# Kernel optimization log

Hardware: AMD Instinct MI355X
Metric: run time of the kernel (lower is better)

## Reference

```python
import jax, jax.numpy as jnp
import numpy as np

B, N, E, H = 8, 512, 64, 128


def setup_inputs() -> dict:
    key = jax.random.key(0)
    ks = jax.random.split(key, 9)
    s_in = 1.0 / np.sqrt(2 * E)
    s_h = 1.0 / np.sqrt(H)
    s_e = 1.0 / np.sqrt(E)
    return {
        "X": jax.random.normal(ks[0], (B, N, E), dtype=jnp.float32),
        # cross-sim MLP: Linear(2E,H) -> ReLU -> Linear(H,1) -> Sigmoid
        "Wc1": jax.random.uniform(ks[1], (2 * E, H), jnp.float32, -s_in, s_in),
        "bc1": jax.random.uniform(ks[2], (H,), jnp.float32, -s_in, s_in),
        "Wc2": jax.random.uniform(ks[3], (H, 1), jnp.float32, -s_h, s_h),
        "bc2": jax.random.uniform(ks[4], (1,), jnp.float32, -s_h, s_h),
        # self-sim MLP: Linear(E,H) -> ReLU -> Linear(H,1) -> Sigmoid
        "Ws1": jax.random.uniform(ks[5], (E, H), jnp.float32, -s_e, s_e),
        "bs1": jax.random.uniform(ks[6], (H,), jnp.float32, -s_e, s_e),
        "Ws2": jax.random.uniform(ks[7], (H, 1), jnp.float32, -s_h, s_h),
        "bs2": jax.random.uniform(ks[8], (1,), jnp.float32, -s_h, s_h),
    }


def reference(X, Wc1, bc1, Wc2, bc2, Ws1, bs1, Ws2, bs2):
    b, n, _ = X.shape
    idx_i, idx_j = jnp.triu_indices(n, k=1)  # [P], P = n(n-1)/2

    # gather pairwise features: [B, P, 2E]
    X_i = X[:, idx_i, :]
    X_j = X[:, idx_j, :]
    pair = jnp.concatenate([X_i, X_j], axis=-1)

    # tiny cross-sim MLP -> [B, P]
    h = jax.nn.relu(jnp.einsum("bpe,eh->bph", pair, Wc1) + bc1)
    sim_upper = jax.nn.sigmoid(jnp.einsum("bph,ho->bpo", h, Wc2) + bc2)[..., 0]

    # self-sim MLP on the diagonal -> [B, N]
    hd = jax.nn.relu(jnp.einsum("bne,eh->bnh", X, Ws1) + bs1)
    sim_diag = jax.nn.sigmoid(jnp.einsum("bnh,ho->bno", hd, Ws2) + bs2)[..., 0]

    # scatter into symmetric sim matrix [B, N, N]
    sim = jnp.zeros((b, n, n), dtype=X.dtype)
    sim = sim.at[:, idx_i, idx_j].set(sim_upper)
    sim = sim.at[:, idx_j, idx_i].set(sim_upper)
    diag = jnp.arange(n)
    sim = sim.at[:, diag, diag].set(sim_diag)
    return sim
```

## Files before the change

### kernel.cpp

```cpp
#include <hip/hip_runtime.h>

typedef float v4f __attribute__((ext_vector_type(4)));
typedef float v2f __attribute__((ext_vector_type(2)));

#define NTOK 512
#define EDIM 64
#define HDIM 128
#define NN   (NTOK*NTOK)

__device__ __forceinline__ float sigf(float x) {
    return __builtin_amdgcn_rcpf(1.f + __expf(-x));
}

__global__ __launch_bounds__(128) void precomp_kernel(
    const float* __restrict__ X, const float* __restrict__ Wc1, const float* __restrict__ bc1,
    const float* __restrict__ Ws1, const float* __restrict__ bs1,
    const float* __restrict__ Ws2, const float* __restrict__ bs2,
    float* __restrict__ Ag, float* __restrict__ Bg, float* __restrict__ out)
{
    __shared__ float Xs[8*EDIM];
    __shared__ float red[8*132];
    const int t  = threadIdx.x;
    const int g0 = blockIdx.x * 8;

    for (int i = t; i < 8*EDIM; i += 128) Xs[i] = X[g0*EDIM + i];
    __syncthreads();

    float accA[8] = {0}, accB[8] = {0}, accS[8] = {0};
    #pragma unroll 8
    for (int e = 0; e < EDIM; e++) {
        float wt = Wc1[e*HDIM + t];
        float wb = Wc1[(EDIM+e)*HDIM + t];
        float ws = Ws1[e*HDIM + t];
        #pragma unroll
        for (int r = 0; r < 8; r++) {
            float x = Xs[r*EDIM + e];
            accA[r] = fmaf(x, wt, accA[r]);
            accB[r] = fmaf(x, wb, accB[r]);
            accS[r] = fmaf(x, ws, accS[r]);
        }
    }
    const float b1 = bc1[t], s1 = bs1[t], w2 = Ws2[t];
    #pragma unroll
    for (int r = 0; r < 8; r++) {
        Ag[(g0+r)*HDIM + t] = accA[r];
        Bg[(g0+r)*HDIM + t] = accB[r] + b1;
        float hd = fmaxf(accS[r] + s1, 0.f);
        red[r*132 + t] = hd * w2;
    }
    __syncthreads();
    if (t < 8) {
        const float* rr = red + t*132;
        float s = 0.f;
        #pragma unroll
        for (int i = 0; i < HDIM/4; i++) {
            v4f v = *(const v4f*)(rr + 4*i);
            s += v[0] + v[1] + v[2] + v[3];
        }
        float val = sigf(s + bs2[0]);
        int g = g0 + t;
        int b = g >> 9, n = g & 511;
        out[b*NN + n*NTOK + n] = val;
    }
}

__global__ __launch_bounds__(256) void pair_kernel(
    const float* __restrict__ Ag, const float* __restrict__ Bg,
    const float* __restrict__ Wc2, const float* __restrict__ bc2,
    float* __restrict__ out)
{
    __shared__ float RowT[64*HDIM];
    __shared__ float ColT[32*HDIM];
    __shared__ float WcS[HDIM];

    const int t = threadIdx.x;
    const int b = blockIdx.y;
    const int u = blockIdx.x;
    int tr, tc, half;
    if (u < 56) {
        int p = u >> 1; half = u & 1;
        tr = 0; int rem = p;
        while (rem >= 7 - tr) { rem -= 7 - tr; tr++; }
        tc = tr + 1 + rem;
    } else {
        int d = (u - 56) >> 1; half = u & 1; tr = d; tc = d;
    }
    const int r0 = tr*64, c0 = tc*64 + half*32;
    const bool isdiag = (tr == tc);

    const float* Rsrc = Ag + (b*NTOK + r0)*HDIM;
    const float* Csrc = Bg + (b*NTOK + c0)*HDIM;

    if (t < 32) *(v4f*)(WcS + 4*t) = *(const v4f*)(Wc2 + 4*t);
    {
        const int hv = t & 31;
        for (int k = t >> 5; k < 64; k += 8) {
            const int sw = 4*(hv ^ (k & 31));
            *(v4f*)(RowT + k*HDIM + sw) = *(const v4f*)(Rsrc + k*HDIM + 4*hv);
        }
        for (int k = t >> 5; k < 32; k += 8) {
            const int sw = 4*(hv ^ k);
            *(v4f*)(ColT + k*HDIM + sw) = *(const v4f*)(Csrc + k*HDIM + 4*hv);
        }
    }
    __syncthreads();

    const int tj = t & 15, ti = t >> 4;
    int rbase[4], rmask[4];
    #pragma unroll
    for (int uu = 0; uu < 4; uu++) { int k = ti + 16*uu; rbase[uu] = k*HDIM; rmask[uu] = k & 31; }
    int cbase[2], cmask[2];
    #pragma unroll
    for (int v = 0; v < 2; v++) { int c = 2*tj + v; cbase[v] = c*HDIM; cmask[v] = c & 31; }

    float acc[4][2] = {};
    for (int hq = 0; hq < HDIM/4; hq++) {
        const v4f w4 = *(const v4f*)(WcS + 4*hq);
        v4f ra[4], cb[2];
        #pragma unroll
        for (int uu = 0; uu < 4; uu++) ra[uu] = *(const v4f*)(RowT + rbase[uu] + 4*(hq ^ rmask[uu]));
        #pragma unroll
        for (int v = 0; v < 2; v++)   cb[v]  = *(const v4f*)(ColT + cbase[v] + 4*(hq ^ cmask[v]));
        #pragma unroll
        for (int hh = 0; hh < 4; hh++) {
            #pragma unroll
            for (int uu = 0; uu < 4; uu++) {
                #pragma unroll
                for (int v = 0; v < 2; v++) {
                    float s = fmaxf(ra[uu][hh] + cb[v][hh], 0.f);
                    acc[uu][v] = fmaf(s, w4[hh], acc[uu][v]);
                }
            }
        }
    }

    const float bb = bc2[0];
    float* outb = out + b*NN;
    float sv[4][2];
    #pragma unroll
    for (int uu = 0; uu < 4; uu++)
        #pragma unroll
        for (int v = 0; v < 2; v++) sv[uu][v] = sigf(acc[uu][v] + bb);

    if (!isdiag) {
        #pragma unroll
        for (int uu = 0; uu < 4; uu++) {
            int r = r0 + ti + 16*uu;
            v2f p; p[0] = sv[uu][0]; p[1] = sv[uu][1];
            *(v2f*)(outb + r*NTOK + c0 + 2*tj) = p;
        }
        __syncthreads();
        float* Tb = ColT;
        #pragma unroll
        for (int uu = 0; uu < 4; uu++)
            #pragma unroll
            for (int v = 0; v < 2; v++)
                Tb[(2*tj + v)*68 + ti + 16*uu] = sv[uu][v];
        __syncthreads();
        const int q = t >> 3, x0 = (t & 7) * 8;
        const float* src = Tb + q*68 + x0;
        v4f a0 = *(const v4f*)src;
        v4f a1 = *(const v4f*)(src + 4);
        float* drow = outb + (c0 + q)*NTOK + r0 + x0;
        *(v4f*)drow = a0;
        *(v4f*)(drow + 4) = a1;
    } else {
        #pragma unroll
        for (int uu = 0; uu < 4; uu++) {
            int r = r0 + ti + 16*uu;
            #pragma unroll
            for (int v = 0; v < 2; v++) {
                int c = c0 + 2*tj + v;
                if (r < c) {
                    outb[r*NTOK + c] = sv[uu][v];
                    outb[c*NTOK + r] = sv[uu][v];
                }
            }
        }
    }
}

extern "C" void kernel_launch(void* const* d_in, const int* in_sizes, int n_in,
                              void* d_out, int out_size, void* d_ws, size_t ws_size,
                              hipStream_t stream) {
    const float* X   = (const float*)d_in[0];
    const float* Wc1 = (const float*)d_in[1];
    const float* bc1 = (const float*)d_in[2];
    const float* Wc2 = (const float*)d_in[3];
    const float* bc2 = (const float*)d_in[4];
    const float* Ws1 = (const float*)d_in[5];
    const float* bs1 = (const float*)d_in[6];
    const float* Ws2 = (const float*)d_in[7];
    const float* bs2 = (const float*)d_in[8];
    float* out = (float*)d_out;

    float* Ag = (float*)d_ws;
    float* Bg = Ag + 8*NTOK*HDIM;

    precomp_kernel<<<dim3(4096/8), dim3(128), 0, stream>>>(X, Wc1, bc1, Ws1, bs1, Ws2, bs2, Ag, Bg, out);
    pair_kernel<<<dim3(72, 8), dim3(256), 0, stream>>>(Ag, Bg, Wc2, bc2, out);
}
```

Measured before the change: 104.5 us.

## Transpose column tile in LDS and use packed v2f math in pair kernel

```diff
diff --git a/kernel.cpp b/kernel.cpp
--- a/kernel.cpp
+++ b/kernel.cpp
@@ -7,6 +7,7 @@
 #define EDIM 64
 #define HDIM 128
 #define NN   (NTOK*NTOK)
+#define CPAD 36
 
 __device__ __forceinline__ float sigf(float x) {
     return __builtin_amdgcn_rcpf(1.f + __expf(-x));
@@ -70,8 +71,7 @@
     float* __restrict__ out)
 {
     __shared__ float RowT[64*HDIM];
-    __shared__ float ColT[32*HDIM];
-    __shared__ float WcS[HDIM];
+    __shared__ float ColT[HDIM*CPAD];
 
     const int t = threadIdx.x;
     const int b = blockIdx.y;
@@ -91,71 +91,87 @@
     const float* Rsrc = Ag + (b*NTOK + r0)*HDIM;
     const float* Csrc = Bg + (b*NTOK + c0)*HDIM;
 
-    if (t < 32) *(v4f*)(WcS + 4*t) = *(const v4f*)(Wc2 + 4*t);
     {
         const int hv = t & 31;
         for (int k = t >> 5; k < 64; k += 8) {
             const int sw = 4*(hv ^ (k & 31));
             *(v4f*)(RowT + k*HDIM + sw) = *(const v4f*)(Rsrc + k*HDIM + 4*hv);
         }
-        for (int k = t >> 5; k < 32; k += 8) {
-            const int sw = 4*(hv ^ k);
-            *(v4f*)(ColT + k*HDIM + sw) = *(const v4f*)(Csrc + k*HDIM + 4*hv);
+        for (int c = t >> 5; c < 32; c += 8) {
+            #pragma unroll
+            for (int e = 0; e < 4; e++) {
+                int h = hv + 32*e;
+                ColT[h*CPAD + c] = Csrc[c*HDIM + h];
+            }
         }
     }
     __syncthreads();
 
-    const int tj = t & 15, ti = t >> 4;
-    int rbase[4], rmask[4];
-    #pragma unroll
-    for (int uu = 0; uu < 4; uu++) { int k = ti + 16*uu; rbase[uu] = k*HDIM; rmask[uu] = k & 31; }
-    int cbase[2], cmask[2];
-    #pragma unroll
-    for (int v = 0; v < 2; v++) { int c = 2*tj + v; cbase[v] = c*HDIM; cmask[v] = c & 31; }
-
-    float acc[4][2] = {};
+    const int w  = t >> 6;
+    const int wr = w & 1, wc = w >> 1;
+    const int l  = t & 63;
+    const int ri = l & 15, cj = l >> 4;
+    const int row0 = 32*wr + ri;
+    const int ccol = 16*wc + 4*cj;
+
+    const int rb0 = row0*HDIM,      rm0 = row0 & 31;
+    const int rb1 = (row0+16)*HDIM, rm1 = (row0+16) & 31;
+
+    v2f acc[2][2] = {{{0,0},{0,0}},{{0,0},{0,0}}};
     for (int hq = 0; hq < HDIM/4; hq++) {
-        const v4f w4 = *(const v4f*)(WcS + 4*hq);
-        v4f ra[4], cb[2];
-        #pragma unroll
-        for (int uu = 0; uu < 4; uu++) ra[uu] = *(const v4f*)(RowT + rbase[uu] + 4*(hq ^ rmask[uu]));
-        #pragma unroll
-        for (int v = 0; v < 2; v++)   cb[v]  = *(const v4f*)(ColT + cbase[v] + 4*(hq ^ cmask[v]));
+        const v4f w4 = *(const v4f*)(Wc2 + 4*hq);
+        v4f ra0 = *(const v4f*)(RowT + rb0 + 4*(hq ^ rm0));
+        v4f ra1 = *(const v4f*)(RowT + rb1 + 4*(hq ^ rm1));
         #pragma unroll
         for (int hh = 0; hh < 4; hh++) {
-            #pragma unroll
-            for (int uu = 0; uu < 4; uu++) {
-                #pragma unroll
-                for (int v = 0; v < 2; v++) {
-                    float s = fmaxf(ra[uu][hh] + cb[v][hh], 0.f);
-                    acc[uu][v] = fmaf(s, w4[hh], acc[uu][v]);
-                }
+            const v4f cb = *(const v4f*)(ColT + (4*hq+hh)*CPAD + ccol);
+            v2f clo; clo[0] = cb[0]; clo[1] = cb[1];
+            v2f chi; chi[0] = cb[2]; chi[1] = cb[3];
+            const float wv = w4[hh];
+            v2f wv2; wv2[0] = wv; wv2[1] = wv;
+            v2f z = {0.f, 0.f};
+            {
+                v2f a2; a2[0] = ra0[hh]; a2[1] = ra0[hh];
+                v2f y0 = __builtin_elementwise_max(a2 + clo, z);
+                v2f y1 = __builtin_elementwise_max(a2 + chi, z);
+                acc[0][0] += y0 * wv2;
+                acc[0][1] += y1 * wv2;
+            }
+            {
+                v2f a2; a2[0] = ra1[hh]; a2[1] = ra1[hh];
+                v2f y0 = __builtin_elementwise_max(a2 + clo, z);
+                v2f y1 = __builtin_elementwise_max(a2 + chi, z);
+                acc[1][0] += y0 * wv2;
+                acc[1][1] += y1 * wv2;
             }
         }
     }
 
     const float bb = bc2[0];
     float* outb = out + b*NN;
-    float sv[4][2];
+    float sv[2][4];
     #pragma unroll
-    for (int uu = 0; uu < 4; uu++)
-        #pragma unroll
-        for (int v = 0; v < 2; v++) sv[uu][v] = sigf(acc[uu][v] + bb);
+    for (int uu = 0; uu < 2; uu++) {
+        sv[uu][0] = sigf(acc[uu][0][0] + bb);
+        sv[uu][1] = sigf(acc[uu][0][1] + bb);
+        sv[uu][2] = sigf(acc[uu][1][0] + bb);
+        sv[uu][3] = sigf(acc[uu][1][1] + bb);
+    }
 
     if (!isdiag) {
         #pragma unroll
-        for (int uu = 0; uu < 4; uu++) {
-            int r = r0 + ti + 16*uu;
-            v2f p; p[0] = sv[uu][0]; p[1] = sv[uu][1];
-            *(v2f*)(outb + r*NTOK + c0 + 2*tj) = p;
+        for (int uu = 0; uu < 2; uu++) {
+            int r = r0 + row0 + 16*uu;
+            v4f p; p[0] = sv[uu][0]; p[1] = sv[uu][1]; p[2] = sv[uu][2]; p[3] = sv[uu][3];
+            *(v4f*)(outb + r*NTOK + c0 + ccol) = p;
         }
         __syncthreads();
         float* Tb = ColT;
         #pragma unroll
-        for (int uu = 0; uu < 4; uu++)
+        for (int uu = 0; uu < 2; uu++)
             #pragma unroll
-            for (int v = 0; v < 2; v++)
-                Tb[(2*tj + v)*68 + ti + 16*uu] = sv[uu][v];
+            for (int v = 0; v < 4; v++)
+                Tb[(ccol + v)*68 + row0 + 16*uu] = sv[uu][v];
         __syncthreads();
         const int q = t >> 3, x0 = (t & 7) * 8;
         const float* src = Tb + q*68 + x0;
@@ -166,11 +182,11 @@
         *(v4f*)(drow + 4) = a1;
     } else {
         #pragma unroll
-        for (int uu = 0; uu < 4; uu++) {
-            int r = r0 + ti + 16*uu;
+        for (int uu = 0; uu < 2; uu++) {
+            int r = r0 + row0 + 16*uu;
             #pragma unroll
-            for (int v = 0; v < 2; v++) {
-                int c = c0 + 2*tj + v;
+            for (int v = 0; v < 4; v++) {
+                int c = c0 + ccol + v;
                 if (r < c) {
                     outb[r*NTOK + c] = sv[uu][v];
                     outb[c*NTOK + r] = sv[uu][v];
```

Result: no change. 103.4 us (-1.0%).
